# Optimization experiments

Hardware: AMD Instinct MI355X
Metric: run time of the kernel (lower is better)

## Reference

```python
import jax, jax.numpy as jnp
import numpy as np

NUM_OBJ = 3
MIN_OBJ_SCALE = 0.1
MAX_OBJ_SCALE = 0.8
MIN_Y_SCALE = 0.75
MAX_Y_SCALE = 1.25
OBJ_POS_BOUND = 0.9
EPS_FIX = 0.095
BIG = 1e12


def setup_inputs() -> dict:
    key = jax.random.key(0)
    k1, k2, k3 = jax.random.split(key, 3)
    n, T, C, H, W = 64, 32, 3, 64, 64
    x = jax.random.normal(k1, (n, T, C, H, W), dtype=jnp.float32)
    d = C * H * W
    W_enc = jax.random.normal(k2, (d, NUM_OBJ * 8), dtype=jnp.float32) / np.sqrt(d).astype(np.float32)
    b_enc = jax.random.normal(k3, (NUM_OBJ * 8,), dtype=jnp.float32) * 0.01
    return {"x": x, "W_enc": W_enc, "b_enc": b_enc}


def _constrain_zp_mean(zp):
    # zp: (nTo, 8) -> mean (nTo, 4). std branch is discarded by forward().
    zm = jnp.concatenate([jax.nn.sigmoid(zp[:, 0:2]), 2.0 * jax.nn.sigmoid(zp[:, 2:4]) - 1.0], -1)
    set_max = jnp.array([[MAX_OBJ_SCALE - MIN_OBJ_SCALE, MAX_Y_SCALE - MIN_Y_SCALE, OBJ_POS_BOUND, OBJ_POS_BOUND]], dtype=zp.dtype)
    set_min = jnp.array([[MIN_OBJ_SCALE, MIN_Y_SCALE, 0.0, 0.0]], dtype=zp.dtype)
    return zm * set_max + set_min


def _greedy_assign(errors):
    # errors: (n, o, o). Greedy row-by-row argmin, masking out used columns with BIG,
    # exactly as the torch fault-fix loop does via scatter of 1e12.
    n, o, _ = errors.shape
    def step(used, i):
        e = errors[:, i, :] + used * BIG
        j = jnp.argmin(e, -1)
        used = used + jax.nn.one_hot(j, o, dtype=errors.dtype)
        return used, j
    _, js = jax.lax.scan(step, jnp.zeros((n, o), errors.dtype), jnp.arange(o))
    return jnp.moveaxis(js, 0, 1)  # (n, o)


def _match_objects(z):
    # z: (n, T, o, 4). Sequential greedy matching over time.
    def step(prev, z_t):
        curr = jax.lax.stop_gradient(z_t[:, :, 2:4])          # (n, o, 2)
        prv = jax.lax.stop_gradient(prev[:, :, 2:4])          # (n, o, 2)
        errors = jnp.sum((prv[:, :, None, :] - curr[:, None, :, :]) ** 2, -1)  # (n, i, j)
        idx = jnp.argmin(errors, -1)                          # (n, o)
        # fault = assignment is not a permutation (num_obj==3 check from source)
        ok = jnp.all(idx[:, 1:] != idx[:, :-1], -1) & (idx[:, 0] != idx[:, 2])
        gidx = _greedy_assign(errors)
        idx = jnp.where(ok[:, None], idx, gidx)
        match = jnp.take_along_axis(z_t, idx[:, :, None], axis=1)
        return match, match
    z0 = z[:, 0]
    _, rest = jax.lax.scan(step, z0, jnp.moveaxis(z[:, 1:], 1, 0))
    return jnp.concatenate([z0[:, None], jnp.moveaxis(rest, 0, 1)], 1)


def _fix_supair(z):
    # z: (n, T, o, 4). Replace isolated position jumps with neighbor average.
    n, T, o, d = z.shape
    diffs = jax.lax.stop_gradient(jnp.abs(z[:, 1:, :, :2] - z[:, :-1, :, :2]))
    zpad2 = jnp.zeros((n, 1, o, 2), z.dtype)
    prev = jnp.concatenate([zpad2, diffs], 1)
    after = jnp.concatenate([diffs, zpad2], 1)
    mask = (prev > EPS_FIX) & (after > EPS_FIX)               # (n, T, o, 2)
    zpad = jnp.zeros((n, 1, o, d), z.dtype)
    smooth = jnp.concatenate([zpad, (z[:, :-2] + z[:, 2:]) / 2, zpad], 1)
    mask_full = jnp.concatenate((d // 2) * [mask], -1)        # (n, T, o, 4)
    return jnp.where(mask_full, smooth, z)


def reference(x, W_enc, b_enc):
    n, T = x.shape[0], x.shape[1]
    # encoder: per-frame linear to (num_obj, 8) z-parameters
    zp = x.reshape(n * T, -1) @ W_enc + b_enc                  # (nT, o*8)
    zm = _constrain_zp_mean(zp.reshape(-1, 8))                 # (nTo, 4)
    z = zm.reshape(n, T, NUM_OBJ, 4)
    z = _match_objects(z)
    z = _fix_supair(z)
    # v_from_state
    v = z[:, 1:, :, 2:] - z[:, :-1, :, 2:]
    zf = jnp.concatenate([z[:, 1:], v], -1)                    # (n, T-1, o, 6)
    zf = jnp.concatenate([jnp.zeros_like(zf[:, 0:1]), zf], 1)  # (n, T, o, 6)
    zf = zf[:, 1:, :, 2:]                                      # (n, T-1, o, 4)
    zf = jnp.concatenate([(zf[..., :2] + 1) / 2 * 10, zf[..., 2:] / 2 * 10], -1)
    zf = jnp.concatenate([zf[..., :2] / 5, zf[..., 2:] * 2], -1)
    return zf
```

## Files before the change

### kernel.cpp

```cpp
#include <hip/hip_runtime.h>

#define N_B   64
#define T_S   32
#define DIM   12288
#define ROWS  2048
#define NCOL  12
#define RPBK  64
#define KB    128
#define KSPL  (DIM / KB)
#define XSTR  133

typedef float f4 __attribute__((ext_vector_type(4)));

__global__ __launch_bounds__(256) void k_gemm(const float* __restrict__ x,
                                              const float* __restrict__ W,
                                              float* __restrict__ part) {
    __shared__ float xs[RPBK * XSTR];
    const int bx  = blockIdx.x;
    const int rg  = bx / KSPL;
    const int sg  = bx - rg * KSPL;
    const int tid = threadIdx.x;
    const int r0  = rg * RPBK;
    const int kb0 = sg * KB;

#pragma unroll
    for (int it = 0; it < 8; ++it) {
        const int flat = tid + it * 256;
        const int row  = flat >> 5;
        const int c4   = flat & 31;
        const f4 v = *(const f4*)(x + (size_t)(r0 + row) * DIM + kb0 + c4 * 4);
        *(f4*)(xs + row * XSTR + c4 * 4) = v;
    }
    __syncthreads();

    const int w    = __builtin_amdgcn_readfirstlane(tid >> 6);
    const int lane = tid & 63;

    f4 xr[8];
#pragma unroll
    for (int i = 0; i < 8; ++i)
        xr[i] = *(const f4*)(xs + lane * XSTR + w * 32 + i * 4);

    float acc[NCOL];
#pragma unroll
    for (int c = 0; c < NCOL; ++c) acc[c] = 0.f;

    const float* wbase = W + (size_t)(kb0 + w * 32) * 24;
#pragma unroll
    for (int i = 0; i < 8; ++i) {
#pragma unroll
        for (int kk = 0; kk < 4; ++kk) {
            const float  xv = xr[i][kk];
            const float* wr = wbase + (i * 4 + kk) * 24;
            acc[0]  += xv * wr[0];  acc[1]  += xv * wr[1];
            acc[2]  += xv * wr[2];  acc[3]  += xv * wr[3];
            acc[4]  += xv * wr[8];  acc[5]  += xv * wr[9];
            acc[6]  += xv * wr[10]; acc[7]  += xv * wr[11];
            acc[8]  += xv * wr[16]; acc[9]  += xv * wr[17];
            acc[10] += xv * wr[18]; acc[11] += xv * wr[19];
        }
    }
    __syncthreads();

#pragma unroll
    for (int c = 0; c < NCOL; ++c)
        xs[w * (64 * 13) + lane * 13 + c] = acc[c];
    __syncthreads();

#pragma unroll
    for (int j = 0; j < 3; ++j) {
        const int i   = tid + j * 256;
        const int row = i / NCOL;
        const int c   = i - row * NCOL;
        float s = 0.f;
#pragma unroll
        for (int ww = 0; ww < 4; ++ww)
            s += xs[ww * (64 * 13) + row * 13 + c];
        part[(size_t)sg * (ROWS * NCOL) + (size_t)rg * (RPBK * NCOL) + i] = s;
    }
}

__global__ __launch_bounds__(256) void k_reduce(const float* __restrict__ part,
                                                const float* __restrict__ b_enc,
                                                float* __restrict__ zbuf) {
    const int rc = blockIdx.x * 256 + threadIdx.x;
    float s = 0.f;
#pragma unroll 8
    for (int i = 0; i < KSPL; ++i) s += part[(size_t)i * (ROWS * NCOL) + rc];

    const int row = rc / NCOL;
    const int c   = rc - row * NCOL;
    const int o   = c >> 2;
    const int cp  = c & 3;
    s += b_enc[o * 8 + cp];
    const float sg = 1.f / (1.f + expf(-s));
    float v;
    if (cp == 0)      v = sg * 0.7f + 0.1f;
    else if (cp == 1) v = sg * 0.5f + 0.75f;
    else              v = (2.f * sg - 1.f) * 0.9f;
    zbuf[rc] = v;
}

__global__ __launch_bounds__(64) void k_post(const float* __restrict__ zbuf,
                                             float* __restrict__ out) {
    __shared__ float z[T_S * NCOL];
    __shared__ float zm[T_S * NCOL];
    __shared__ float zf[T_S * NCOL];
    __shared__ int   perm[T_S];
    const int b   = blockIdx.x;
    const int tid = threadIdx.x;

#pragma unroll
    for (int i = 0; i < 6; ++i)
        z[tid + 64 * i] = zbuf[b * 384 + tid + 64 * i];
    __syncthreads();

    if (tid == 0) {
        float px0 = z[2],  py0 = z[3];
        float px1 = z[6],  py1 = z[7];
        float px2 = z[10], py2 = z[11];
        for (int t = 1; t < T_S; ++t) {
            const int base = t * 12;
            const float cx0 = z[base + 2],  cy0 = z[base + 3];
            const float cx1 = z[base + 6],  cy1 = z[base + 7];
            const float cx2 = z[base + 10], cy2 = z[base + 11];

            float dx, dy;
            dx = px0 - cx0; dy = py0 - cy0; const float e00 = dx * dx + dy * dy;
            dx = px0 - cx1; dy = py0 - cy1; const float e01 = dx * dx + dy * dy;
            dx = px0 - cx2; dy = py0 - cy2; const float e02 = dx * dx + dy * dy;
            dx = px1 - cx0; dy = py1 - cy0; const float e10 = dx * dx + dy * dy;
            dx = px1 - cx1; dy = py1 - cy1; const float e11 = dx * dx + dy * dy;
            dx = px1 - cx2; dy = py1 - cy2; const float e12 = dx * dx + dy * dy;
            dx = px2 - cx0; dy = py2 - cy0; const float e20 = dx * dx + dy * dy;
            dx = px2 - cx1; dy = py2 - cy1; const float e21 = dx * dx + dy * dy;
            dx = px2 - cx2; dy = py2 - cy2; const float e22 = dx * dx + dy * dy;

            auto amin3 = [](float a0, float a1, float a2) {
                int j = 0; float e = a0;
                if (a1 < e) { e = a1; j = 1; }
                if (a2 < e) { j = 2; }
                return j;
            };
            int i0 = amin3(e00, e01, e02);
            int i1 = amin3(e10, e11, e12);
            int i2 = amin3(e20, e21, e22);
            const bool ok = (i1 != i0) && (i2 != i1) && (i0 != i2);
            if (!ok) {
                float u0 = 0.f, u1 = 0.f, u2 = 0.f;
                i0 = amin3(e00, e01, e02);
                if (i0 == 0) u0 = 1.f; else if (i0 == 1) u1 = 1.f; else u2 = 1.f;
                i1 = amin3(e10 + u0 * 1e12f, e11 + u1 * 1e12f, e12 + u2 * 1e12f);
                if (i1 == 0) u0 = 1.f; else if (i1 == 1) u1 = 1.f; else u2 = 1.f;
                i2 = amin3(e20 + u0 * 1e12f, e21 + u1 * 1e12f, e22 + u2 * 1e12f);
            }
            perm[t] = i0 * 9 + i1 * 3 + i2;
            px0 = (i0 == 0) ? cx0 : (i0 == 1) ? cx1 : cx2;
            py0 = (i0 == 0) ? cy0 : (i0 == 1) ? cy1 : cy2;
            px1 = (i1 == 0) ? cx0 : (i1 == 1) ? cx1 : cx2;
            py1 = (i1 == 0) ? cy0 : (i1 == 1) ? cy1 : cy2;
            px2 = (i2 == 0) ? cx0 : (i2 == 1) ? cx1 : cx2;
            py2 = (i2 == 0) ? cy0 : (i2 == 1) ? cy1 : cy2;
        }
    }
    __syncthreads();

#pragma unroll
    for (int ii = 0; ii < 6; ++ii) {
        const int i  = tid + 64 * ii;
        const int t  = i / 12;
        const int j  = i - t * 12;
        const int k  = j >> 2;
        const int ch = j & 3;
        int p = k;
        if (t > 0) {
            const int code = perm[t];
            p = (k == 0) ? code / 9 : (k == 1) ? (code % 9) / 3 : code % 3;
        }
        zm[i] = z[t * 12 + p * 4 + ch];
    }
    __syncthreads();

#pragma unroll
    for (int ii = 0; ii < 6; ++ii) {
        const int i  = tid + 64 * ii;
        const int t  = i / 12;
        const int j  = i - t * 12;
        const int o  = j >> 2;
        const int cc = j & 1;
        const int mb = o * 4 + cc;
        const float pd = (t >= 1)  ? fabsf(zm[t * 12 + mb] - zm[(t - 1) * 12 + mb]) : 0.f;
        const float ad = (t <= 30) ? fabsf(zm[(t + 1) * 12 + mb] - zm[t * 12 + mb]) : 0.f;
        const bool  m  = (pd > 0.095f) && (ad > 0.095f);
        const float sm = (t >= 1 && t <= 30)
                             ? (zm[(t - 1) * 12 + j] + zm[(t + 1) * 12 + j]) * 0.5f
                             : 0.f;
        zf[i] = m ? sm : zm[t * 12 + j];
    }
    __syncthreads();

    for (int i = tid; i < 31 * 12; i += 64) {
        const int t  = i / 12;
        const int j  = i - t * 12;
        const int o  = j >> 2;
        const int c2 = j & 3;
        const int pb = o * 4 + 2 + (c2 & 1);
        float v;
        if (c2 < 2) v = zf[(t + 1) * 12 + pb] + 1.f;
        else        v = (zf[(t + 1) * 12 + pb] - zf[t * 12 + pb]) * 10.f;
        out[b * 372 + i] = v;
    }
}

extern "C" void kernel_launch(void* const* d_in, const int* in_sizes, int n_in,
                              void* d_out, int out_size, void* d_ws, size_t ws_size,
                              hipStream_t stream) {
    (void)in_sizes; (void)n_in; (void)out_size; (void)ws_size;
    const float* x     = (const float*)d_in[0];
    const float* W_enc = (const float*)d_in[1];
    const float* b_enc = (const float*)d_in[2];
    float* out  = (float*)d_out;

    float* zbuf = (float*)d_ws;
    float* part = zbuf + ROWS * NCOL;

    k_gemm  <<<(ROWS / RPBK) * KSPL, 256, 0, stream>>>(x, W_enc, part);
    k_reduce<<<(ROWS * NCOL) / 256, 256, 0, stream>>>(part, b_enc, zbuf);
    k_post  <<<N_B, 64, 0, stream>>>(zbuf, out);
}
```

Before: 176.6 us.

## Loop k_gemm over six K subtiles with double-buffered LDS prefetch

The GEMM kernel now processes a 768-wide K slab per block, looping over six 128-wide subtiles. It prefetches the next x tile into registers while computing on the current one, using two LDS buffers. This cuts the split-K factor from 96 to 16, which shrinks the partial-sum buffer and the work left for the reduce kernel. In exchange there are far fewer blocks (512 instead of 3072) and LDS use doubles, which may lower occupancy and latency hiding.

```diff
diff --git a/kernel.cpp b/kernel.cpp
--- a/kernel.cpp
+++ b/kernel.cpp
@@ -6,8 +6,9 @@
 #define ROWS  2048
 #define NCOL  12
 #define RPBK  64
-#define KB    128
-#define KSPL  (DIM / KB)
+#define KSPL  16
+#define KSLAB 768
+#define NSUB  6
 #define XSTR  133
 
 typedef float f4 __attribute__((ext_vector_type(4)));
@@ -15,56 +16,71 @@
 __global__ __launch_bounds__(256) void k_gemm(const float* __restrict__ x,
                                               const float* __restrict__ W,
                                               float* __restrict__ part) {
-    __shared__ float xs[RPBK * XSTR];
-    const int bx  = blockIdx.x;
-    const int rg  = bx / KSPL;
-    const int sg  = bx - rg * KSPL;
-    const int tid = threadIdx.x;
-    const int r0  = rg * RPBK;
-    const int kb0 = sg * KB;
-
-#pragma unroll
-    for (int it = 0; it < 8; ++it) {
-        const int flat = tid + it * 256;
-        const int row  = flat >> 5;
-        const int c4   = flat & 31;
-        const f4 v = *(const f4*)(x + (size_t)(r0 + row) * DIM + kb0 + c4 * 4);
-        *(f4*)(xs + row * XSTR + c4 * 4) = v;
-    }
-    __syncthreads();
-
-    const int w    = __builtin_amdgcn_readfirstlane(tid >> 6);
+    __shared__ float xs[2][RPBK * XSTR];
+    const int rg   = blockIdx.x >> 4;
+    const int sg   = blockIdx.x & 15;
+    const int tid  = threadIdx.x;
+    const int wave = tid >> 6;
     const int lane = tid & 63;
-
-    f4 xr[8];
-#pragma unroll
-    for (int i = 0; i < 8; ++i)
-        xr[i] = *(const f4*)(xs + lane * XSTR + w * 32 + i * 4);
+    const int r0   = rg * RPBK;
+    const int kb   = sg * KSLAB;
+    const int srow = tid >> 5;
+    const int sc4  = tid & 31;
+
+    f4 xv[8];
+
+#define LOAD_TILE(t)                                                          \
+    _Pragma("unroll")                                                         \
+    for (int i = 0; i < 8; ++i)                                               \
+        xv[i] = *(const f4*)(x + (size_t)(r0 + srow + i * 8) * DIM            \
+                               + kb + (t) * 128 + sc4 * 4);
+
+#define WRITE_TILE(b)                                                         \
+    _Pragma("unroll")                                                         \
+    for (int i = 0; i < 8; ++i)                                               \
+        *(f4*)(&xs[b][(srow + i * 8) * XSTR + sc4 * 4]) = xv[i];
 
     float acc[NCOL];
 #pragma unroll
     for (int c = 0; c < NCOL; ++c) acc[c] = 0.f;
 
-    const float* wbase = W + (size_t)(kb0 + w * 32) * 24;
-#pragma unroll
-    for (int i = 0; i < 8; ++i) {
-#pragma unroll
-        for (int kk = 0; kk < 4; ++kk) {
-            const float  xv = xr[i][kk];
-            const float* wr = wbase + (i * 4 + kk) * 24;
-            acc[0]  += xv * wr[0];  acc[1]  += xv * wr[1];
-            acc[2]  += xv * wr[2];  acc[3]  += xv * wr[3];
-            acc[4]  += xv * wr[8];  acc[5]  += xv * wr[9];
-            acc[6]  += xv * wr[10]; acc[7]  += xv * wr[11];
-            acc[8]  += xv * wr[16]; acc[9]  += xv * wr[17];
-            acc[10] += xv * wr[18]; acc[11] += xv * wr[19];
-        }
-    }
-    __syncthreads();
-
+    LOAD_TILE(0)
+    WRITE_TILE(0)
+    __syncthreads();
+
+#pragma unroll
+    for (int t = 0; t < NSUB; ++t) {
+        if (t < NSUB - 1) { LOAD_TILE(t + 1) }
+
+        const float* wb   = W + (size_t)(kb + t * 128 + wave * 32) * 24;
+        const float* xrow = &xs[t & 1][lane * XSTR + wave * 32];
+#pragma unroll
+        for (int i = 0; i < 8; ++i) {
+            const f4 xr = *(const f4*)(xrow + i * 4);
+#pragma unroll
+            for (int kk = 0; kk < 4; ++kk) {
+                const float  xvs = xr[kk];
+                const float* wr  = wb + (i * 4 + kk) * 24;
+                acc[0]  += xvs * wr[0];  acc[1]  += xvs * wr[1];
+                acc[2]  += xvs * wr[2];  acc[3]  += xvs * wr[3];
+                acc[4]  += xvs * wr[8];  acc[5]  += xvs * wr[9];
+                acc[6]  += xvs * wr[10]; acc[7]  += xvs * wr[11];
+                acc[8]  += xvs * wr[16]; acc[9]  += xvs * wr[17];
+                acc[10] += xvs * wr[18]; acc[11] += xvs * wr[19];
+            }
+        }
+
+        if (t < NSUB - 1) {
+            WRITE_TILE((t + 1) & 1)
+            __syncthreads();
+        }
+    }
+    __syncthreads();
+
+    float* pk = &xs[0][0];
 #pragma unroll
     for (int c = 0; c < NCOL; ++c)
-        xs[w * (64 * 13) + lane * 13 + c] = acc[c];
+        pk[wave * (64 * 13) + lane * 13 + c] = acc[c];
     __syncthreads();
 
 #pragma unroll
@@ -74,10 +90,12 @@
         const int c   = i - row * NCOL;
         float s = 0.f;
 #pragma unroll
-        for (int ww = 0; ww < 4; ++ww)
-            s += xs[ww * (64 * 13) + row * 13 + c];
+        for (int w = 0; w < 4; ++w)
+            s += pk[w * (64 * 13) + row * 13 + c];
         part[(size_t)sg * (ROWS * NCOL) + (size_t)rg * (RPBK * NCOL) + i] = s;
     }
+#undef LOAD_TILE
+#undef WRITE_TILE
 }
 
 __global__ __launch_bounds__(256) void k_reduce(const float* __restrict__ part,
@@ -85,7 +103,7 @@
                                                 float* __restrict__ zbuf) {
     const int rc = blockIdx.x * 256 + threadIdx.x;
     float s = 0.f;
-#pragma unroll 8
+#pragma unroll
     for (int i = 0; i < KSPL; ++i) s += part[(size_t)i * (ROWS * NCOL) + rc];
 
     const int row = rc / NCOL;
```

Result: slower. 213.7 us (+21.0%).
